# Performance work log

Measured on AMD Instinct MI355X. Metric: run time of the kernel, lower is better.

## Reference

```python
import jax, jax.numpy as jnp
import numpy as np

B, S, DM, H, DK, DH = 8, 1024, 512, 8, 32, 64
LN_EPS = 1e-5
NEG_SLOPE = 0.01  # torch LeakyReLU default


def _l2norm(t, axis=-1, eps=1e-12):
    # matches F.normalize(p=2): x / max(||x||, eps)
    n = jnp.sqrt(jnp.sum(t * t, axis=axis, keepdims=True))
    return t / jnp.maximum(n, eps)


def _layernorm(t, w, b, eps=LN_EPS):
    mu = jnp.mean(t, axis=-1, keepdims=True)
    var = jnp.mean((t - mu) ** 2, axis=-1, keepdims=True)
    return (t - mu) * jax.lax.rsqrt(var + eps) * w + b


def setup_inputs() -> dict:
    key = jax.random.key(0)
    ks = jax.random.split(key, 16)
    x = jax.random.normal(ks[0], (B, S, DM), dtype=jnp.float32)
    # causal-style mask: True = masked (upper triangle)
    attn_mask = jnp.broadcast_to(jnp.triu(jnp.ones((S, S), dtype=bool), k=1), (B, S, S))
    pairwise_dist = jax.random.uniform(ks[1], (B, S, S), dtype=jnp.float32)
    s = 0.02
    return {
        "x": x,
        "attn_mask": attn_mask,
        "pairwise_dist": pairwise_dist,
        "Wq": jax.random.normal(ks[2], (H, DK, DM), dtype=jnp.float32) * s,
        "Wk": jax.random.normal(ks[3], (H, DK, DM), dtype=jnp.float32) * s,
        "Wv": jax.random.normal(ks[4], (H, DH, DM), dtype=jnp.float32) * s,
        "omega": jnp.ones((H,), dtype=jnp.float32),
        "Wo": jax.random.normal(ks[5], (DM, H * DH), dtype=jnp.float32) * s,
        "bo": jnp.zeros((DM,), dtype=jnp.float32),
        "Wf": jax.random.normal(ks[6], (DM, DM), dtype=jnp.float32) * s,
        "bf": jnp.zeros((DM,), dtype=jnp.float32),
        "ln1_w": jnp.ones((DM,), dtype=jnp.float32),
        "ln1_b": jnp.zeros((DM,), dtype=jnp.float32),
        "ln2_w": jnp.ones((DM,), dtype=jnp.float32),
        "ln2_b": jnp.zeros((DM,), dtype=jnp.float32),
    }


def _encoder_layer(x, attn_mask, pairwise_dist, Wq, Wk, Wv, omega,
                   Wo, bo, Wf, bf, ln1_w, ln1_b, ln2_w, ln2_b):
    # --- multi-head self-attention, all heads batched ---
    q = _l2norm(jnp.einsum('bsd,hkd->hbsk', x, Wq))   # [H,B,S,DK]
    k = _l2norm(jnp.einsum('bsd,hkd->hbsk', x, Wk))
    v = jnp.einsum('bsd,hvd->hbsv', x, Wv)            # [H,B,S,DH]
    scores = jnp.einsum('hbsk,hbtk->hbst', q, k)      # cosine-sim, [H,B,S,S]
    # distance bias: exp(-omega*d) - 1, detached in the original
    r = jax.lax.stop_gradient(
        jnp.exp(-omega[:, None, None, None] * pairwise_dist[None]) - 1.0)
    scores = scores + r
    scores = jnp.where(attn_mask[None], -jnp.inf, scores)
    # custom softmax: exp(x) / (sum + 1); exp(-inf)=0 handles masking
    z = jnp.exp(scores)
    attn = z / (jnp.sum(z, axis=-1, keepdims=True) + 1.0)
    y = jnp.einsum('hbst,hbtv->hbsv', attn, v)        # [H,B,S,DH]
    y = jnp.transpose(y, (1, 2, 0, 3)).reshape(x.shape[0], x.shape[1], -1)  # concat heads
    x_attn = y @ Wo.T + bo
    # --- residual + LN + FFN (dropout p=0 -> identity) ---
    z1 = _layernorm(x + x_attn, ln1_w, ln1_b)
    z_ff = jax.nn.leaky_relu(z1 @ Wf.T + bf, negative_slope=NEG_SLOPE)
    return _layernorm(z1 + z_ff, ln2_w, ln2_b)


def reference(x, attn_mask, pairwise_dist, Wq, Wk, Wv, omega,
              Wo, bo, Wf, bf, ln1_w, ln1_b, ln2_w, ln2_b):
    return _encoder_layer(x, attn_mask, pairwise_dist, Wq, Wk, Wv, omega,
                          Wo, bo, Wf, bf, ln1_w, ln1_b, ln2_w, ln2_b)
```

## Files before the change

### kernel.cpp

```cpp
#include <hip/hip_runtime.h>
#include <hip/hip_bf16.h>
#include <math.h>

#define BB 8
#define SS 1024
#define DMM 512
#define HH 8
#define DKK 32
#define DHH 64

typedef __bf16 bf16x8 __attribute__((ext_vector_type(8)));
typedef float f32x4 __attribute__((ext_vector_type(4)));

template <int MODE>
__global__ __launch_bounds__(256) void gemm_mfma(
    const float* __restrict__ A, const float* __restrict__ W0,
    const float* __restrict__ W1, const float* __restrict__ W2,
    const float* __restrict__ bias, const float* __restrict__ resid,
    float* __restrict__ C, int N) {
  __shared__ __bf16 As[128][40];
  __shared__ __bf16 Bs[128][40];

  const int tid = threadIdx.x;
  const int n0 = blockIdx.x * 128;
  const int m0 = blockIdx.y * 128;

  const float* Wt;
  int nofs;
  if (MODE == 0) {
    if (n0 < 256) { Wt = W0; nofs = n0; }
    else if (n0 < 512) { Wt = W1; nofs = n0 - 256; }
    else { Wt = W2; nofs = n0 - 512; }
  } else {
    Wt = W0; nofs = n0;
  }

  const int lane = tid & 63;
  const int w = tid >> 6;
  const int wm = (w & 1) * 64;
  const int wn = (w >> 1) * 64;
  const int fr = lane & 15;
  const int fk = (lane >> 4) * 8;

  f32x4 acc[4][4];
#pragma unroll
  for (int mi = 0; mi < 4; ++mi)
#pragma unroll
    for (int ni = 0; ni < 4; ++ni) acc[mi][ni] = (f32x4){0.f, 0.f, 0.f, 0.f};

  for (int kt = 0; kt < 512; kt += 32) {
    __syncthreads();
#pragma unroll
    for (int i = 0; i < 4; ++i) {
      int q = tid + i * 256;
      int r = q >> 3, k4 = (q & 7) * 4;
      float4 av = *(const float4*)&A[(size_t)(m0 + r) * 512 + kt + k4];
      float4 bv = *(const float4*)&Wt[(size_t)(nofs + r) * 512 + kt + k4];
      union { __hip_bfloat162 h2[2]; uint2 u; } pa, pb;
      pa.h2[0] = __float22bfloat162_rn(make_float2(av.x, av.y));
      pa.h2[1] = __float22bfloat162_rn(make_float2(av.z, av.w));
      pb.h2[0] = __float22bfloat162_rn(make_float2(bv.x, bv.y));
      pb.h2[1] = __float22bfloat162_rn(make_float2(bv.z, bv.w));
      *(uint2*)&As[r][k4] = pa.u;
      *(uint2*)&Bs[r][k4] = pb.u;
    }
    __syncthreads();

    bf16x8 af[4], bf[4];
#pragma unroll
    for (int mi = 0; mi < 4; ++mi)
      af[mi] = *(const bf16x8*)&As[wm + mi * 16 + fr][fk];
#pragma unroll
    for (int ni = 0; ni < 4; ++ni)
      bf[ni] = *(const bf16x8*)&Bs[wn + ni * 16 + fr][fk];
#pragma unroll
    for (int mi = 0; mi < 4; ++mi)
#pragma unroll
      for (int ni = 0; ni < 4; ++ni)
        acc[mi][ni] = __builtin_amdgcn_mfma_f32_16x16x32_bf16(
            af[mi], bf[ni], acc[mi][ni], 0, 0, 0);
  }

  const int er = (lane >> 4) * 4;
  const int ec = lane & 15;
#pragma unroll
  for (int mi = 0; mi < 4; ++mi) {
#pragma unroll
    for (int ni = 0; ni < 4; ++ni) {
      const int n = n0 + wn + ni * 16 + ec;
      float bsv = (MODE != 0) ? bias[n] : 0.0f;
#pragma unroll
      for (int r = 0; r < 4; ++r) {
        const int m = m0 + wm + mi * 16 + er + r;
        float v = acc[mi][ni][r];
        if (MODE == 1) {
          v += bsv + resid[(size_t)m * 512 + n];
        } else if (MODE == 2) {
          float g = v + bsv;
          g = g > 0.f ? g : 0.01f * g;
          v = resid[(size_t)m * 512 + n] + g;
        }
        C[(size_t)m * N + n] = v;
      }
    }
  }
}

__global__ __launch_bounds__(256) void prep_qkv(
    const float* __restrict__ qkv, __bf16* __restrict__ Qg,
    __bf16* __restrict__ Kg, __bf16* __restrict__ Vt) {
  __shared__ __bf16 vt[64][136];
  const int bh = blockIdx.x;
  const int b = bh >> 3, h = bh & 7;
  const int sb = blockIdx.y * 128;
  const int tid = threadIdx.x;

  {
    const int row = tid >> 1, half = tid & 1;
    const size_t rb = ((size_t)b * 1024 + sb + row) * 1024;
    {
      const float* p = qkv + rb + h * 32 + half * 16;
      float4 a[4];
      float ss = 0.f;
#pragma unroll
      for (int i = 0; i < 4; ++i) {
        a[i] = ((const float4*)p)[i];
        ss += a[i].x * a[i].x + a[i].y * a[i].y + a[i].z * a[i].z + a[i].w * a[i].w;
      }
      ss += __shfl_xor(ss, 1, 64);
      float sc = 1.0f / fmaxf(sqrtf(ss), 1e-12f);
      union { __hip_bfloat162 h2[4]; uint4 u; } pk[2];
#pragma unroll
      for (int i = 0; i < 2; ++i) {
        pk[i].h2[0] = __float22bfloat162_rn(make_float2(a[2*i].x * sc, a[2*i].y * sc));
        pk[i].h2[1] = __float22bfloat162_rn(make_float2(a[2*i].z * sc, a[2*i].w * sc));
        pk[i].h2[2] = __float22bfloat162_rn(make_float2(a[2*i+1].x * sc, a[2*i+1].y * sc));
        pk[i].h2[3] = __float22bfloat162_rn(make_float2(a[2*i+1].z * sc, a[2*i+1].w * sc));
      }
      uint4* o = (uint4*)(Qg + ((size_t)bh * 1024 + sb + row) * 32 + half * 16);
      o[0] = pk[0].u; o[1] = pk[1].u;
    }
    {
      const float* p = qkv + rb + 256 + h * 32 + half * 16;
      float4 a[4];
      float ss = 0.f;
#pragma unroll
      for (int i = 0; i < 4; ++i) {
        a[i] = ((const float4*)p)[i];
        ss += a[i].x * a[i].x + a[i].y * a[i].y + a[i].z * a[i].z + a[i].w * a[i].w;
      }
      ss += __shfl_xor(ss, 1, 64);
      float sc = 1.0f / fmaxf(sqrtf(ss), 1e-12f);
      union { __hip_bfloat162 h2[4]; uint4 u; } pk[2];
#pragma unroll
      for (int i = 0; i < 2; ++i) {
        pk[i].h2[0] = __float22bfloat162_rn(make_float2(a[2*i].x * sc, a[2*i].y * sc));
        pk[i].h2[1] = __float22bfloat162_rn(make_float2(a[2*i].z * sc, a[2*i].w * sc));
        pk[i].h2[2] = __float22bfloat162_rn(make_float2(a[2*i+1].x * sc, a[2*i+1].y * sc));
        pk[i].h2[3] = __float22bfloat162_rn(make_float2(a[2*i+1].z * sc, a[2*i+1].w * sc));
      }
      uint4* o = (uint4*)(Kg + ((size_t)bh * 1024 + sb + row) * 32 + half * 16);
      o[0] = pk[0].u; o[1] = pk[1].u;
    }
  }

#pragma unroll
  for (int i = 0; i < 8; ++i) {
    int idx = tid + i * 256;
    int t = idx >> 4, vd4 = (idx & 15) * 4;
    float4 v = *(const float4*)&qkv[((size_t)b * 1024 + sb + t) * 1024 + 512 + h * 64 + vd4];
    vt[vd4 + 0][t] = (__bf16)v.x;
    vt[vd4 + 1][t] = (__bf16)v.y;
    vt[vd4 + 2][t] = (__bf16)v.z;
    vt[vd4 + 3][t] = (__bf16)v.w;
  }
  __syncthreads();
  {
    const int vd = tid >> 2, tseg = (tid & 3) * 32;
    uint4* o = (uint4*)(Vt + (size_t)bh * 65536 + (size_t)vd * 1024 + sb + tseg);
#pragma unroll
    for (int j = 0; j < 4; ++j)
      o[j] = *(const uint4*)&vt[vd][tseg + j * 8];
  }
}

__global__ __launch_bounds__(256) void attn_mfma(
    const __bf16* __restrict__ Qg, const __bf16* __restrict__ Kg,
    const __bf16* __restrict__ Vt, const float* __restrict__ dist,
    const float* __restrict__ omega, float* __restrict__ y) {
  __shared__ __bf16 Qs[64 * 32];
  __shared__ __bf16 Ks[64 * 32];
  __shared__ __bf16 Vs[64 * 64];
  __shared__ __bf16 zs[64][72];

  const int b = blockIdx.x;
  const int s0 = (15 - blockIdx.y) * 64;
  const int h = blockIdx.z;
  const int bh = b * 8 + h;
  const int tid = threadIdx.x;
  const int lane = tid & 63;
  const int w = tid >> 6;
  const int quad = lane >> 4;
  const int m = lane & 15;
  const float om = omega[h];
  const size_t rowbase = (size_t)b * SS;

  {
    int row = tid >> 2, p = tid & 3;
    uint4 v = *(const uint4*)(Qg + ((size_t)bh * 1024 + s0 + row) * 32 + p * 8);
    *(uint4*)&Qs[row * 32 + ((p ^ ((row >> 1) & 3)) * 8)] = v;
  }

  const int kswz = (quad ^ ((m >> 1) & 3)) * 8;
  const int sl = 16 * w + m;

  f32x4 acc[4];
#pragma unroll
  for (int ni = 0; ni < 4; ++ni) acc[ni] = (f32x4){0.f, 0.f, 0.f, 0.f};
  float zsum = 0.0f;
  const int ntiles = (s0 >> 6) + 1;

  for (int tt = 0; tt < ntiles; ++tt) {
    const int t0 = tt * 64;
    __syncthreads();
    {
      int row = tid >> 2, p = tid & 3;
      uint4 v = *(const uint4*)(Kg + ((size_t)bh * 1024 + t0 + row) * 32 + p * 8);
      *(uint4*)&Ks[row * 32 + ((p ^ ((row >> 1) & 3)) * 8)] = v;
    }
#pragma unroll
    for (int i = 0; i < 2; ++i) {
      int idx = tid + i * 256;
      int vd = idx >> 3, p = idx & 7;
      uint4 v = *(const uint4*)(Vt + (size_t)bh * 65536 + (size_t)vd * 1024 + t0 + p * 8);
      *(uint4*)&Vs[vd * 64 + ((p ^ (vd & 7)) * 8)] = v;
    }
    float4 dv[4];
#pragma unroll
    for (int mi = 0; mi < 4; ++mi)
      dv[mi] = *(const float4*)&dist[(rowbase + s0 + sl) * SS + t0 + 16 * mi + quad * 4];
    __syncthreads();

    const bf16x8 bq = *(const bf16x8*)&Qs[sl * 32 + kswz];
    f32x4 sc4[4];
#pragma unroll
    for (int mi = 0; mi < 4; ++mi) {
      const bf16x8 ak = *(const bf16x8*)&Ks[(16 * mi + m) * 32 + kswz];
      sc4[mi] = __builtin_amdgcn_mfma_f32_16x16x32_bf16(
          ak, bq, (f32x4){0.f, 0.f, 0.f, 0.f}, 0, 0, 0);
    }
    const bool diag = (tt == ntiles - 1);
#pragma unroll
    for (int mi = 0; mi < 4; ++mi) {
      float zr[4];
#pragma unroll
      for (int r = 0; r < 4; ++r) {
        float d = (&dv[mi].x)[r];
        float zv = __expf(sc4[mi][r] + __expf(-om * d) - 1.0f);
        if (diag && (16 * mi + quad * 4 + r) > sl) zv = 0.0f;
        zr[r] = zv;
        zsum += zv;
      }
      union { __hip_bfloat162 h2[2]; uint2 u; } pz;
      pz.h2[0] = __float22bfloat162_rn(make_float2(zr[0], zr[1]));
      pz.h2[1] = __float22bfloat162_rn(make_float2(zr[2], zr[3]));
      *(uint2*)&zs[sl][16 * mi + quad * 4] = pz.u;
    }
    __syncthreads();

    const bf16x8 za0 = *(const bf16x8*)&zs[sl][quad * 8];
    const bf16x8 za1 = *(const bf16x8*)&zs[sl][quad * 8 + 32];
#pragma unroll
    for (int ni = 0; ni < 4; ++ni) {
      const bf16x8 vb0 = *(const bf16x8*)&Vs[(16 * ni + m) * 64 + ((quad ^ (m & 7)) * 8)];
      const bf16x8 vb1 = *(const bf16x8*)&Vs[(16 * ni + m) * 64 + (((quad + 4) ^ (m & 7)) * 8)];
      acc[ni] = __builtin_amdgcn_mfma_f32_16x16x32_bf16(za0, vb0, acc[ni], 0, 0, 0);
      acc[ni] = __builtin_amdgcn_mfma_f32_16x16x32_bf16(za1, vb1, acc[ni], 0, 0, 0);
    }
  }

  zsum += __shfl_xor(zsum, 16, 64);
  zsum += __shfl_xor(zsum, 32, 64);

#pragma unroll
  for (int r = 0; r < 4; ++r) {
    float dn = __shfl(zsum, quad * 4 + r, 64);
    float inv = 1.0f / (dn + 1.0f);
    float* yp = &y[(rowbase + s0 + 16 * w + quad * 4 + r) * 512 + h * 64 + m];
#pragma unroll
    for (int ni = 0; ni < 4; ++ni)
      yp[16 * ni] = acc[ni][r] * inv;
  }
}

__global__ __launch_bounds__(256) void ln_kernel(
    const float* __restrict__ in, const float* __restrict__ w,
    const float* __restrict__ bvec, float* __restrict__ out) {
  __shared__ float sbuf[4];
  const int m = blockIdx.x;
  const int tid = threadIdx.x;
  const float2 v = ((const float2*)(in + (size_t)m * 512))[tid];
  float s = v.x + v.y;
#pragma unroll
  for (int off = 32; off > 0; off >>= 1) s += __shfl_down(s, off, 64);
  const int lane = tid & 63, wid = tid >> 6;
  if (lane == 0) sbuf[wid] = s;
  __syncthreads();
  const float mu = (sbuf[0] + sbuf[1] + sbuf[2] + sbuf[3]) * (1.0f / 512.0f);
  __syncthreads();
  const float dx = v.x - mu, dy = v.y - mu;
  float s2 = dx * dx + dy * dy;
#pragma unroll
  for (int off = 32; off > 0; off >>= 1) s2 += __shfl_down(s2, off, 64);
  if (lane == 0) sbuf[wid] = s2;
  __syncthreads();
  const float var = (sbuf[0] + sbuf[1] + sbuf[2] + sbuf[3]) * (1.0f / 512.0f);
  const float inv = rsqrtf(var + 1e-5f);
  const float2 wv = ((const float2*)w)[tid];
  const float2 bv = ((const float2*)bvec)[tid];
  float2 o;
  o.x = dx * inv * wv.x + bv.x;
  o.y = dy * inv * wv.y + bv.y;
  ((float2*)(out + (size_t)m * 512))[tid] = o;
}

extern "C" void kernel_launch(void* const* d_in, const int* in_sizes, int n_in,
                              void* d_out, int out_size, void* d_ws, size_t ws_size,
                              hipStream_t stream) {
  const float* x = (const float*)d_in[0];
  const float* dist = (const float*)d_in[2];
  const float* Wq = (const float*)d_in[3];
  const float* Wk = (const float*)d_in[4];
  const float* Wv = (const float*)d_in[5];
  const float* omega = (const float*)d_in[6];
  const float* Wo = (const float*)d_in[7];
  const float* bo = (const float*)d_in[8];
  const float* Wf = (const float*)d_in[9];
  const float* bf_ = (const float*)d_in[10];
  const float* ln1w = (const float*)d_in[11];
  const float* ln1b = (const float*)d_in[12];
  const float* ln2w = (const float*)d_in[13];
  const float* ln2b = (const float*)d_in[14];
  float* out = (float*)d_out;

  float* ws = (float*)d_ws;
  float* qkv = ws;
  float* ybuf = ws;
  float* t1 = ws + (size_t)4 * 1024 * 1024;
  __bf16* Qg = (__bf16*)(ws + (size_t)8 * 1024 * 1024);
  __bf16* Kg = Qg + (size_t)2 * 1024 * 1024;
  __bf16* Vt = Kg + (size_t)2 * 1024 * 1024;
  float* h2 = ws + (size_t)8 * 1024 * 1024;

  dim3 blk(256);
  gemm_mfma<0><<<dim3(8, 64), blk, 0, stream>>>(x, Wq, Wk, Wv, nullptr, nullptr,
                                                qkv, 1024);
  prep_qkv<<<dim3(64, 8), blk, 0, stream>>>(qkv, Qg, Kg, Vt);
  attn_mfma<<<dim3(8, 16, 8), blk, 0, stream>>>(Qg, Kg, Vt, dist, omega, ybuf);
  gemm_mfma<1><<<dim3(4, 64), blk, 0, stream>>>(ybuf, Wo, nullptr, nullptr, bo, x,
                                                t1, 512);
  ln_kernel<<<dim3(8192), blk, 0, stream>>>(t1, ln1w, ln1b, t1);
  gemm_mfma<2><<<dim3(4, 64), blk, 0, stream>>>(t1, Wf, nullptr, nullptr, bf_, t1,
                                                h2, 512);
  ln_kernel<<<dim3(8192), blk, 0, stream>>>(h2, ln2w, ln2b, out);
}
```

Before: 278.5 us.

## Pre-convert GEMM operands to bf16 and load tiles via direct global-to-LDS

Adds conversion kernels that turn x and the weight matrices into bf16 buffers. The GEMMs now read bf16 operands and copy tiles straight into swizzled LDS with global_load_lds, so they no longer convert on the fly through registers. The attention output and the LN1 output are also written in bf16 to halve the bytes the next GEMM reads. The cost is three extra conversion launches per call and a rearranged workspace in which several buffers alias one another.

```diff
diff --git a/kernel.cpp b/kernel.cpp
--- a/kernel.cpp
+++ b/kernel.cpp
@@ -1,6 +1,7 @@
 #include <hip/hip_runtime.h>
 #include <hip/hip_bf16.h>
 #include <math.h>
+#include <stdint.h>
 
 #define BB 8
 #define SS 1024
@@ -12,35 +13,75 @@
 typedef __bf16 bf16x8 __attribute__((ext_vector_type(8)));
 typedef float f32x4 __attribute__((ext_vector_type(4)));
 
+__device__ __forceinline__ void gll16(const void* g, void* l) {
+  __builtin_amdgcn_global_load_lds(
+      (const __attribute__((address_space(1))) void*)(uintptr_t)g,
+      (__attribute__((address_space(3))) void*)(uint32_t)(uintptr_t)l,
+      16, 0, 0);
+}
+
+__device__ __forceinline__ uint4 pack8(const float4 a, const float4 b) {
+  union { __hip_bfloat162 h2[4]; uint4 u; } p;
+  p.h2[0] = __float22bfloat162_rn(make_float2(a.x, a.y));
+  p.h2[1] = __float22bfloat162_rn(make_float2(a.z, a.w));
+  p.h2[2] = __float22bfloat162_rn(make_float2(b.x, b.y));
+  p.h2[3] = __float22bfloat162_rn(make_float2(b.z, b.w));
+  return p.u;
+}
+
+__global__ __launch_bounds__(256) void cvt_f32_bf16(
+    const float* __restrict__ s, __bf16* __restrict__ d) {
+  size_t i = ((size_t)blockIdx.x * 256 + threadIdx.x) * 8;
+  float4 a = *(const float4*)&s[i];
+  float4 b = *(const float4*)&s[i + 4];
+  *(uint4*)&d[i] = pack8(a, b);
+}
+
+__global__ __launch_bounds__(256) void cvt_wqkv(
+    const float* __restrict__ Wq, const float* __restrict__ Wk,
+    const float* __restrict__ Wv, __bf16* __restrict__ d) {
+  size_t i = ((size_t)blockIdx.x * 256 + threadIdx.x) * 8;
+  const float* s;
+  size_t off;
+  if (i < 131072) { s = Wq; off = i; }
+  else if (i < 262144) { s = Wk; off = i - 131072; }
+  else { s = Wv; off = i - 262144; }
+  float4 a = *(const float4*)&s[off];
+  float4 b = *(const float4*)&s[off + 4];
+  *(uint4*)&d[i] = pack8(a, b);
+}
+
+__global__ __launch_bounds__(256) void cvt_wof(
+    const float* __restrict__ Wo, const float* __restrict__ Wf,
+    __bf16* __restrict__ dWo, __bf16* __restrict__ dWf) {
+  size_t i = ((size_t)blockIdx.x * 256 + threadIdx.x) * 8;
+  const float* s;
+  __bf16* d;
+  size_t off;
+  if (i < 262144) { s = Wo; d = dWo; off = i; }
+  else { s = Wf; d = dWf; off = i - 262144; }
+  float4 a = *(const float4*)&s[off];
+  float4 b = *(const float4*)&s[off + 4];
+  *(uint4*)&d[off] = pack8(a, b);
+}
+
 template <int MODE>
-__global__ __launch_bounds__(256) void gemm_mfma(
-    const float* __restrict__ A, const float* __restrict__ W0,
-    const float* __restrict__ W1, const float* __restrict__ W2,
+__global__ __launch_bounds__(256) void gemm_bf16(
+    const __bf16* __restrict__ A, const __bf16* __restrict__ W,
     const float* __restrict__ bias, const float* __restrict__ resid,
     float* __restrict__ C, int N) {
-  __shared__ __bf16 As[128][40];
-  __shared__ __bf16 Bs[128][40];
-
+  __shared__ __bf16 As[128 * 32];
+  __shared__ __bf16 Bs[128 * 32];
   const int tid = threadIdx.x;
   const int n0 = blockIdx.x * 128;
   const int m0 = blockIdx.y * 128;
-
-  const float* Wt;
-  int nofs;
-  if (MODE == 0) {
-    if (n0 < 256) { Wt = W0; nofs = n0; }
-    else if (n0 < 512) { Wt = W1; nofs = n0 - 256; }
-    else { Wt = W2; nofs = n0 - 512; }
-  } else {
-    Wt = W0; nofs = n0;
-  }
-
   const int lane = tid & 63;
   const int w = tid >> 6;
-  const int wm = (w & 1) * 64;
-  const int wn = (w >> 1) * 64;
-  const int fr = lane & 15;
-  const int fk = (lane >> 4) * 8;
+  const int wm = (w & 1) * 64, wn = (w >> 1) * 64;
+  const int fr = lane & 15, quad = lane >> 4;
+
+  const int srow = lane >> 2;
+  const int schunk = (lane & 3) ^ ((lane >> 3) & 3);
 
   f32x4 acc[4][4];
 #pragma unroll
@@ -51,28 +92,22 @@
   for (int kt = 0; kt < 512; kt += 32) {
     __syncthreads();
 #pragma unroll
-    for (int i = 0; i < 4; ++i) {
-      int q = tid + i * 256;
-      int r = q >> 3, k4 = (q & 7) * 4;
-      float4 av = *(const float4*)&A[(size_t)(m0 + r) * 512 + kt + k4];
-      float4 bv = *(const float4*)&Wt[(size_t)(nofs + r) * 512 + kt + k4];
-      union { __hip_bfloat162 h2[2]; uint2 u; } pa, pb;
-      pa.h2[0] = __float22bfloat162_rn(make_float2(av.x, av.y));
-      pa.h2[1] = __float22bfloat162_rn(make_float2(av.z, av.w));
-      pb.h2[0] = __float22bfloat162_rn(make_float2(bv.x, bv.y));
-      pb.h2[1] = __float22bfloat162_rn(make_float2(bv.z, bv.w));
-      *(uint2*)&As[r][k4] = pa.u;
-      *(uint2*)&Bs[r][k4] = pb.u;
+    for (int j = 0; j < 2; ++j) {
+      const int seg = w * 2 + j;
+      const int row = seg * 16 + srow;
+      gll16(&A[(size_t)(m0 + row) * 512 + kt + schunk * 8], &As[seg * 512]);
+      gll16(&W[(size_t)(n0 + row) * 512 + kt + schunk * 8], &Bs[seg * 512]);
     }
     __syncthreads();
 
     bf16x8 af[4], bf[4];
+    const int rsw = (quad ^ ((fr >> 1) & 3)) * 8;
 #pragma unroll
     for (int mi = 0; mi < 4; ++mi)
-      af[mi] = *(const bf16x8*)&As[wm + mi * 16 + fr][fk];
+      af[mi] = *(const bf16x8*)&As[(wm + mi * 16 + fr) * 32 + rsw];
 #pragma unroll
     for (int ni = 0; ni < 4; ++ni)
-      bf[ni] = *(const bf16x8*)&Bs[wn + ni * 16 + fr][fk];
+      bf[ni] = *(const bf16x8*)&Bs[(wn + ni * 16 + fr) * 32 + rsw];
 #pragma unroll
     for (int mi = 0; mi < 4; ++mi)
 #pragma unroll
@@ -129,16 +164,13 @@
       }
       ss += __shfl_xor(ss, 1, 64);
       float sc = 1.0f / fmaxf(sqrtf(ss), 1e-12f);
-      union { __hip_bfloat162 h2[4]; uint4 u; } pk[2];
-#pragma unroll
-      for (int i = 0; i < 2; ++i) {
-        pk[i].h2[0] = __float22bfloat162_rn(make_float2(a[2*i].x * sc, a[2*i].y * sc));
-        pk[i].h2[1] = __float22bfloat162_rn(make_float2(a[2*i].z * sc, a[2*i].w * sc));
-        pk[i].h2[2] = __float22bfloat162_rn(make_float2(a[2*i+1].x * sc, a[2*i+1].y * sc));
-        pk[i].h2[3] = __float22bfloat162_rn(make_float2(a[2*i+1].z * sc, a[2*i+1].w * sc));
-      }
+      float4 s0 = make_float4(a[0].x * sc, a[0].y * sc, a[0].z * sc, a[0].w * sc);
+      float4 s1 = make_float4(a[1].x * sc, a[1].y * sc, a[1].z * sc, a[1].w * sc);
+      float4 s2 = make_float4(a[2].x * sc, a[2].y * sc, a[2].z * sc, a[2].w * sc);
+      float4 s3 = make_float4(a[3].x * sc, a[3].y * sc, a[3].z * sc, a[3].w * sc);
       uint4* o = (uint4*)(Qg + ((size_t)bh * 1024 + sb + row) * 32 + half * 16);
-      o[0] = pk[0].u; o[1] = pk[1].u;
+      o[0] = pack8(s0, s1);
+      o[1] = pack8(s2, s3);
     }
     {
       const float* p = qkv + rb + 256 + h * 32 + half * 16;
@@ -151,16 +183,13 @@
       }
       ss += __shfl_xor(ss, 1, 64);
       float sc = 1.0f / fmaxf(sqrtf(ss), 1e-12f);
-      union { __hip_bfloat162 h2[4]; uint4 u; } pk[2];
-#pragma unroll
-      for (int i = 0; i < 2; ++i) {
-        pk[i].h2[0] = __float22bfloat162_rn(make_float2(a[2*i].x * sc, a[2*i].y * sc));
-        pk[i].h2[1] = __float22bfloat162_rn(make_float2(a[2*i].z * sc, a[2*i].w * sc));
-        pk[i].h2[2] = __float22bfloat162_rn(make_float2(a[2*i+1].x * sc, a[2*i+1].y * sc));
-        pk[i].h2[3] = __float22bfloat162_rn(make_float2(a[2*i+1].z * sc, a[2*i+1].w * sc));
-      }
+      float4 s0 = make_float4(a[0].x * sc, a[0].y * sc, a[0].z * sc, a[0].w * sc);
+      float4 s1 = make_float4(a[1].x * sc, a[1].y * sc, a[1].z * sc, a[1].w * sc);
+      float4 s2 = make_float4(a[2].x * sc, a[2].y * sc, a[2].z * sc, a[2].w * sc);
+      float4 s3 = make_float4(a[3].x * sc, a[3].y * sc, a[3].z * sc, a[3].w * sc);
       uint4* o = (uint4*)(Kg + ((size_t)bh * 1024 + sb + row) * 32 + half * 16);
-      o[0] = pk[0].u; o[1] = pk[1].u;
+      o[0] = pack8(s0, s1);
+      o[1] = pack8(s2, s3);
     }
   }
 
@@ -187,7 +216,7 @@
 __global__ __launch_bounds__(256) void attn_mfma(
     const __bf16* __restrict__ Qg, const __bf16* __restrict__ Kg,
     const __bf16* __restrict__ Vt, const float* __restrict__ dist,
-    const float* __restrict__ omega, float* __restrict__ y) {
+    const float* __restrict__ omega, __bf16* __restrict__ y) {
   __shared__ __bf16 Qs[64 * 32];
   __shared__ __bf16 Ks[64 * 32];
   __shared__ __bf16 Vs[64 * 64];
@@ -286,16 +315,17 @@
   for (int r = 0; r < 4; ++r) {
     float dn = __shfl(zsum, quad * 4 + r, 64);
     float inv = 1.0f / (dn + 1.0f);
-    float* yp = &y[(rowbase + s0 + 16 * w + quad * 4 + r) * 512 + h * 64 + m];
+    __bf16* yp = &y[(rowbase + s0 + 16 * w + quad * 4 + r) * 512 + h * 64 + m];
 #pragma unroll
     for (int ni = 0; ni < 4; ++ni)
-      yp[16 * ni] = acc[ni][r] * inv;
+      yp[16 * ni] = (__bf16)(acc[ni][r] * inv);
   }
 }
 
 __global__ __launch_bounds__(256) void ln_kernel(
     const float* __restrict__ in, const float* __restrict__ w,
-    const float* __restrict__ bvec, float* __restrict__ out) {
+    const float* __restrict__ bvec, float* __restrict__ out,
+    __bf16* __restrict__ outb) {
   __shared__ float sbuf[4];
   const int m = blockIdx.x;
   const int tid = threadIdx.x;
@@ -322,6 +352,11 @@
   o.x = dx * inv * wv.x + bv.x;
   o.y = dy * inv * wv.y + bv.y;
   ((float2*)(out + (size_t)m * 512))[tid] = o;
+  if (outb) {
+    union { __hip_bfloat162 h2; unsigned u; } p;
+    p.h2 = __float22bfloat162_rn(make_float2(o.x, o.y));
+    *(unsigned*)&outb[(size_t)m * 512 + tid * 2] = p.u;
+  }
 }
 
 extern "C" void kernel_launch(void* const* d_in, const int* in_sizes, int n_in,
@@ -343,24 +378,30 @@
   const float* ln2b = (const float*)d_in[14];
   float* out = (float*)d_out;
 
-  float* ws = (float*)d_ws;
-  float* qkv = ws;
-  float* ybuf = ws;
-  float* t1 = ws + (size_t)4 * 1024 * 1024;
-  __bf16* Qg = (__bf16*)(ws + (size_t)8 * 1024 * 1024);
-  __bf16* Kg = Qg + (size_t)2 * 1024 * 1024;
-  __bf16* Vt = Kg + (size_t)2 * 1024 * 1024;
-  float* h2 = ws + (size_t)8 * 1024 * 1024;
+  char* base = (char*)d_ws;
+  const size_t MB = 1 << 20;
+  float* qkv = (float*)base;
+  __bf16* yb = (__bf16*)base;
+  float* t1 = (float*)(base + 8 * MB);
+  __bf16* t1b = (__bf16*)(base + 24 * MB);
+  __bf16* xb = (__bf16*)(base + 32 * MB);
+  __bf16* Wcat = (__bf16*)(base + 40 * MB);
+  __bf16* Qg = (__bf16*)(base + 32 * MB);
+  __bf16* Kg = (__bf16*)(base + 36 * MB);
+  __bf16* Vt = (__bf16*)(base + 40 * MB);
+  __bf16* Wob = (__bf16*)(base + 32 * MB);
+  __bf16* Wfb = (__bf16*)(base + 32 * MB + 512 * 1024);
 
   dim3 blk(256);
-  gemm_mfma<0><<<dim3(8, 64), blk, 0, stream>>>(x, Wq, Wk, Wv, nullptr, nullptr,
+  cvt_f32_bf16<<<dim3(2048), blk, 0, stream>>>(x, xb);
+  cvt_wqkv<<<dim3(256), blk, 0, stream>>>(Wq, Wk, Wv, Wcat);
+  gemm_bf16<0><<<dim3(8, 64), blk, 0, stream>>>(xb, Wcat, nullptr, nullptr,
                                                 qkv, 1024);
   prep_qkv<<<dim3(64, 8), blk, 0, stream>>>(qkv, Qg, Kg, Vt);
-  attn_mfma<<<dim3(8, 16, 8), blk, 0, stream>>>(Qg, Kg, Vt, dist, omega, ybuf);
-  gemm_mfma<1><<<dim3(4, 64), blk, 0, stream>>>(ybuf, Wo, nullptr, nullptr, bo, x,
-                                                t1, 512);
-  ln_kernel<<<dim3(8192), blk, 0, stream>>>(t1, ln1w, ln1b, t1);
-  gemm_mfma<2><<<dim3(4, 64), blk, 0, stream>>>(t1, Wf, nullptr, nullptr, bf_, t1,
-                                                h2, 512);
-  ln_kernel<<<dim3(8192), blk, 0, stream>>>(h2, ln2w, ln2b, out);
-}
+  attn_mfma<<<dim3(8, 16, 8), blk, 0, stream>>>(Qg, Kg, Vt, dist, omega, yb);
+  cvt_wof<<<dim3(256), blk, 0, stream>>>(Wo, Wf, Wob, Wfb);
+  gemm_bf16<1><<<dim3(4, 64), blk, 0, stream>>>(yb, Wob, bo, x, t1, 512);
+  ln_kernel<<<dim3(8192), blk, 0, stream>>>(t1, ln1w, ln1b, t1, t1b);
+  gemm_bf16<2><<<dim3(4, 64), blk, 0, stream>>>(t1b, Wfb, bf_, t1, out, 512);
+  ln_kernel<<<dim3(8192), blk, 0, stream>>>(out, ln2w, ln2b, out, nullptr);
+}
```

Result: faster. 263.7 us (-5.3%).
